# Kernel optimization log

Hardware: AMD Instinct MI355X
Metric: run time of the kernel (lower is better)

The kernel has to match this reference:

```python
import jax, jax.numpy as jnp
import numpy as np

KNN = 10       # knn_size
TOPK = 4       # top_k_select
H = 4          # num_heads
HID = 64       # edge-MLP hidden dim


def setup_inputs() -> dict:
    key = jax.random.key(0)
    ks = jax.random.split(key, 12)
    B, V, D = 4, 4096, 256
    s = 0.02
    return {
        "voxel_tokens": jax.random.normal(ks[0], (B, V, D), jnp.float32),
        "voxel_coords": jax.random.uniform(ks[1], (B, V, 3), jnp.float32) * 10.0,
        "mask": jnp.ones((B, V), dtype=bool),
        # EdgeScoringMLP: Linear(2D+3 -> 64), Linear(64 -> 1)
        "W1": jax.random.normal(ks[2], (2 * D + 3, HID), jnp.float32) * s,
        "b1": jnp.zeros((HID,), jnp.float32),
        "W2": jax.random.normal(ks[3], (HID, 1), jnp.float32) * s,
        "b2": jnp.zeros((1,), jnp.float32),
        # CrossAttention projections (D -> D)
        "Wq": jax.random.normal(ks[4], (D, D), jnp.float32) * s,
        "bq": jnp.zeros((D,), jnp.float32),
        "Wk": jax.random.normal(ks[5], (D, D), jnp.float32) * s,
        "bk": jnp.zeros((D,), jnp.float32),
        "Wv": jax.random.normal(ks[6], (D, D), jnp.float32) * s,
        "bv": jnp.zeros((D,), jnp.float32),
        "Wo": jax.random.normal(ks[7], (D, D), jnp.float32) * s,
        "bo": jnp.zeros((D,), jnp.float32),
    }


def reference(voxel_tokens, voxel_coords, mask,
              W1, b1, W2, b2, Wq, bq, Wk, bk, Wv, bv, Wo, bo):
    # mask is all-True (Vp == V per batch element), so the original per-batch
    # loop over dynamic voxel counts is an exact vmap over B. Dropouts are in
    # eval mode (identity).
    D = voxel_tokens.shape[-1]
    Dh = D // H

    def single(tok, coo):  # tok: (V, D), coo: (V, 3)
        # --- KNN graph build (squared euclidean; monotonic in true cdist) ---
        sq = jnp.sum(coo * coo, axis=-1)                        # (V,)
        d2 = sq[:, None] + sq[None, :] - 2.0 * (coo @ coo.T)    # (V, V)
        _, knn = jax.lax.top_k(-d2, KNN + 1)                    # smallest dists
        knn = knn[:, 1:]                                        # drop self, (V, KNN)

        # --- edge features: [anchor_tok, neighbor_tok, rel_pos] ---
        nb_tok = tok[knn]                                       # (V, KNN, D)
        rel = coo[knn] - coo[:, None, :]                        # (V, KNN, 3)
        anchor = jnp.broadcast_to(tok[:, None, :], nb_tok.shape)
        ef = jnp.concatenate([anchor, nb_tok, rel], axis=-1)    # (V, KNN, 2D+3)

        # --- edge-MLP scoring + softmax + top-k edge select ---
        sc = (jax.nn.relu(ef @ W1 + b1) @ W2 + b2)[..., 0]      # (V, KNN)
        aw = jax.nn.softmax(sc, axis=-1)
        _, loc = jax.lax.top_k(aw, TOPK)                        # (V, TOPK)
        sel = jnp.take_along_axis(knn, loc, axis=-1)            # (V, TOPK)
        nbr = tok[sel]                                          # (V, TOPK, D)

        # --- cross attention over selected neighbors ---
        Q = (tok @ Wq + bq).reshape(-1, H, Dh)                  # (V, H, Dh)
        K = (nbr @ Wk + bk).reshape(-1, TOPK, H, Dh)            # (V, TOPK, H, Dh)
        Vv = (nbr @ Wv + bv).reshape(-1, TOPK, H, Dh)
        att = jnp.einsum('vhd,vshd->vhs', Q, K) / jnp.sqrt(jnp.float32(Dh))
        w = jax.nn.softmax(att, axis=-1)                        # (V, H, TOPK)
        out = jnp.einsum('vhs,vshd->vhd', w, Vv).reshape(-1, D)
        return out @ Wo + bo                                    # (V, D)

    return jax.vmap(single)(voxel_tokens, voxel_coords)        # (B, V, D)
```

## Files before the change

kernel.cpp:

```cpp
#include <hip/hip_runtime.h>
#include <hip/hip_bf16.h>

#define VV 4096
#define DDIM 256
#define KNN_K 10
#define TK 4

__device__ __forceinline__ float f_sq3(float x, float y, float z) {
    return __fadd_rn(__fadd_rn(__fmul_rn(x, x), __fmul_rn(y, y)), __fmul_rn(z, z));
}
__device__ __forceinline__ float f_dot3(float ax, float ay, float az,
                                        float bx, float by, float bz) {
    float d = __fmul_rn(ax, bx);
    d = __fmaf_rn(ay, by, d);
    d = __fmaf_rn(az, bz, d);
    return d;
}

__global__ void __launch_bounds__(256) an_gemm_kernel(
    const float* __restrict__ tok,
    const float* __restrict__ W1,
    float* __restrict__ AN)
{
    __shared__ float As[16][68];
    __shared__ float Bs[16][68];

    const int mBlock = blockIdx.x * 64;
    const int grp    = blockIdx.y;
    const float* W   = W1 + (size_t)grp * 256 * 64;

    const int tid = threadIdx.x;
    const int tx = tid & 15;
    const int ty = tid >> 4;

    const int ar  = tid >> 2;
    const int ac4 = tid & 3;
    const int br  = tid >> 4;
    const int bc4 = tid & 15;

    float acc[4][4] = {};

    for (int k0 = 0; k0 < 256; k0 += 16) {
        float4 a4 = *(const float4*)&tok[(size_t)(mBlock + ar) * 256 + k0 + ac4 * 4];
        As[ac4 * 4 + 0][ar] = a4.x;
        As[ac4 * 4 + 1][ar] = a4.y;
        As[ac4 * 4 + 2][ar] = a4.z;
        As[ac4 * 4 + 3][ar] = a4.w;
        float4 b4 = *(const float4*)&W[(size_t)(k0 + br) * 64 + bc4 * 4];
        *(float4*)&Bs[br][bc4 * 4] = b4;
        __syncthreads();
        #pragma unroll
        for (int kk = 0; kk < 16; kk++) {
            float4 av = *(const float4*)&As[kk][ty * 4];
            float4 bv4 = *(const float4*)&Bs[kk][tx * 4];
            acc[0][0] = fmaf(av.x, bv4.x, acc[0][0]); acc[0][1] = fmaf(av.x, bv4.y, acc[0][1]);
            acc[0][2] = fmaf(av.x, bv4.z, acc[0][2]); acc[0][3] = fmaf(av.x, bv4.w, acc[0][3]);
            acc[1][0] = fmaf(av.y, bv4.x, acc[1][0]); acc[1][1] = fmaf(av.y, bv4.y, acc[1][1]);
            acc[1][2] = fmaf(av.y, bv4.z, acc[1][2]); acc[1][3] = fmaf(av.y, bv4.w, acc[1][3]);
            acc[2][0] = fmaf(av.z, bv4.x, acc[2][0]); acc[2][1] = fmaf(av.z, bv4.y, acc[2][1]);
            acc[2][2] = fmaf(av.z, bv4.z, acc[2][2]); acc[2][3] = fmaf(av.z, bv4.w, acc[2][3]);
            acc[3][0] = fmaf(av.w, bv4.x, acc[3][0]); acc[3][1] = fmaf(av.w, bv4.y, acc[3][1]);
            acc[3][2] = fmaf(av.w, bv4.z, acc[3][2]); acc[3][3] = fmaf(av.w, bv4.w, acc[3][3]);
        }
        __syncthreads();
    }

    #pragma unroll
    for (int i = 0; i < 4; i++) {
        int m = mBlock + ty * 4 + i;
        float4 o;
        o.x = acc[i][0]; o.y = acc[i][1]; o.z = acc[i][2]; o.w = acc[i][3];
        *(float4*)&AN[(size_t)m * 128 + grp * 64 + tx * 4] = o;
    }
}

__global__ void __launch_bounds__(256) knn_score_kernel(
    const float* __restrict__ AN,
    const float* __restrict__ coords,
    const float* __restrict__ W1,
    const float* __restrict__ b1,
    const float* __restrict__ W2,
    int* __restrict__ sel)
{
    const int q    = blockIdx.x;
    const int b    = q >> 12;
    const int v    = q & 4095;
    const int base = q & ~4095;
    const int tid  = threadIdx.x;
    const int lane = tid & 63;
    const int wave = tid >> 6;
    const float* cb = coords + (size_t)b * VV * 3;

    __shared__ float sval2[2][4];
    __shared__ int   sidx2[2][4];
    __shared__ int   sKnn[KNN_K];
    __shared__ float sA[64];
    __shared__ float sHid[KNN_K][64];
    __shared__ float sSc[KNN_K];

    const float qx = cb[v * 3 + 0];
    const float qy = cb[v * 3 + 1];
    const float qz = cb[v * 3 + 2];
    const float sqq = f_sq3(qx, qy, qz);

    if (tid < 64) sA[tid] = AN[(size_t)q * 128 + tid];

    float d2[16];
    #pragma unroll
    for (int i = 0; i < 16; i++) {
        int j = tid + i * 256;
        float xj = cb[j * 3 + 0], yj = cb[j * 3 + 1], zj = cb[j * 3 + 2];
        float sqj = f_sq3(xj, yj, zj);
        float dt  = f_dot3(qx, qy, qz, xj, yj, zj);
        d2[i] = __fsub_rn(__fadd_rn(sqq, sqj), __fmul_rn(2.0f, dt));
    }

    unsigned used = 0;
    float best = 3.4e38f;
    int   bi   = 0x7fffffff;
    #pragma unroll
    for (int i = 0; i < 16; i++) {
        if (d2[i] < best) { best = d2[i]; bi = tid + i * 256; }
    }

    for (int it = 0; it < 11; it++) {
        float rb = best;
        int   ri = bi;
        #pragma unroll
        for (int off = 1; off < 64; off <<= 1) {
            float v2 = __shfl_xor(rb, off);
            int   i2 = __shfl_xor(ri, off);
            if (v2 < rb || (v2 == rb && i2 < ri)) { rb = v2; ri = i2; }
        }
        const int p = it & 1;
        if (lane == 0) { sval2[p][wave] = rb; sidx2[p][wave] = ri; }
        __syncthreads();
        float fb = sval2[p][0]; int fi = sidx2[p][0];
        #pragma unroll
        for (int w2 = 1; w2 < 4; w2++) {
            float v2 = sval2[p][w2]; int i2 = sidx2[p][w2];
            if (v2 < fb || (v2 == fb && i2 < fi)) { fb = v2; fi = i2; }
        }
        int w = fi & 4095;
        if (it >= 1 && tid == 0) sKnn[it - 1] = w;
        if ((w & 255) == tid) {
            used |= 1u << (w >> 8);
            best = 3.4e38f; bi = 0x7fffffff;
            #pragma unroll
            for (int i = 0; i < 16; i++) {
                if (used & (1u << i)) continue;
                if (d2[i] < best) { best = d2[i]; bi = tid + i * 256; }
            }
        }
    }
    __syncthreads();

    const float qc[3] = {qx, qy, qz};
    for (int idx = tid; idx < KNN_K * 64; idx += 256) {
        int nb = idx >> 6, h = idx & 63;
        int kn = sKnn[nb];
        float acc = __fadd_rn(sA[h], AN[(size_t)(base + kn) * 128 + 64 + h]);
        #pragma unroll
        for (int c = 0; c < 3; c++) {
            float rel = __fsub_rn(cb[kn * 3 + c], qc[c]);
            acc = __fmaf_rn(rel, W1[(512 + c) * 64 + h], acc);
        }
        float hid = __fadd_rn(acc, b1[h]);
        sHid[nb][h] = hid > 0.0f ? hid : 0.0f;
    }
    __syncthreads();

    if (tid < KNN_K) {
        float s = 0.0f;
        for (int h = 0; h < 64; h++)
            s = __fmaf_rn(sHid[tid][h], W2[h], s);
        sSc[tid] = s;
    }
    __syncthreads();

    if (tid == 0) {
        unsigned um = 0;
        #pragma unroll
        for (int s = 0; s < TK; s++) {
            float bests = -3.4e38f; int bj = 0;
            for (int jj = 0; jj < KNN_K; jj++) {
                if (um & (1u << jj)) continue;
                if (sSc[jj] > bests) { bests = sSc[jj]; bj = jj; }
            }
            um |= 1u << bj;
            sel[(size_t)q * TK + s] = base + sKnn[bj];
        }
    }
}

__global__ void __launch_bounds__(256) qkv_gemm_kernel(
    const float* __restrict__ tok,
    const float* __restrict__ Wq, const float* __restrict__ bq,
    const float* __restrict__ Wk, const float* __restrict__ bk,
    const float* __restrict__ Wv, const float* __restrict__ bv,
    float* __restrict__ qkv)
{
    __shared__ float As[16][68];
    __shared__ float Bs[16][68];

    const int mBlock = blockIdx.x * 64;
    const int nBlock = blockIdx.y * 64;
    const int grp = nBlock >> 8;
    const int nIn = nBlock & 255;
    const float* W    = (grp == 0) ? Wq : (grp == 1) ? Wk : Wv;
    const float* bias = (grp == 0) ? bq : (grp == 1) ? bk : bv;

    const int tid = threadIdx.x;
    const int tx = tid & 15;
    const int ty = tid >> 4;

    const int ar  = tid >> 2;
    const int ac4 = tid & 3;
    const int br  = tid >> 4;
    const int bc4 = tid & 15;

    float acc[4][4] = {};

    for (int k0 = 0; k0 < 256; k0 += 16) {
        float4 a4 = *(const float4*)&tok[(size_t)(mBlock + ar) * 256 + k0 + ac4 * 4];
        As[ac4 * 4 + 0][ar] = a4.x;
        As[ac4 * 4 + 1][ar] = a4.y;
        As[ac4 * 4 + 2][ar] = a4.z;
        As[ac4 * 4 + 3][ar] = a4.w;
        float4 b4 = *(const float4*)&W[(size_t)(k0 + br) * 256 + nIn + bc4 * 4];
        *(float4*)&Bs[br][bc4 * 4] = b4;
        __syncthreads();
        #pragma unroll
        for (int kk = 0; kk < 16; kk++) {
            float4 av = *(const float4*)&As[kk][ty * 4];
            float4 bv4 = *(const float4*)&Bs[kk][tx * 4];
            acc[0][0] = fmaf(av.x, bv4.x, acc[0][0]); acc[0][1] = fmaf(av.x, bv4.y, acc[0][1]);
            acc[0][2] = fmaf(av.x, bv4.z, acc[0][2]); acc[0][3] = fmaf(av.x, bv4.w, acc[0][3]);
            acc[1][0] = fmaf(av.y, bv4.x, acc[1][0]); acc[1][1] = fmaf(av.y, bv4.y, acc[1][1]);
            acc[1][2] = fmaf(av.y, bv4.z, acc[1][2]); acc[1][3] = fmaf(av.y, bv4.w, acc[1][3]);
            acc[2][0] = fmaf(av.z, bv4.x, acc[2][0]); acc[2][1] = fmaf(av.z, bv4.y, acc[2][1]);
            acc[2][2] = fmaf(av.z, bv4.z, acc[2][2]); acc[2][3] = fmaf(av.z, bv4.w, acc[2][3]);
            acc[3][0] = fmaf(av.w, bv4.x, acc[3][0]); acc[3][1] = fmaf(av.w, bv4.y, acc[3][1]);
            acc[3][2] = fmaf(av.w, bv4.z, acc[3][2]); acc[3][3] = fmaf(av.w, bv4.w, acc[3][3]);
        }
        __syncthreads();
    }

    #pragma unroll
    for (int i = 0; i < 4; i++) {
        int m = mBlock + ty * 4 + i;
        float4 o;
        o.x = acc[i][0] + bias[nIn + tx * 4 + 0];
        o.y = acc[i][1] + bias[nIn + tx * 4 + 1];
        o.z = acc[i][2] + bias[nIn + tx * 4 + 2];
        o.w = acc[i][3] + bias[nIn + tx * 4 + 3];
        *(float4*)&qkv[(size_t)m * 768 + nBlock + tx * 4] = o;
    }
}

__global__ void __launch_bounds__(256) attn_gather_kernel(
    const float* __restrict__ qkv, const int* __restrict__ sel,
    float* __restrict__ attnout)
{
    const int q = blockIdx.x;
    const int tid = threadIdx.x;

    const float qv = qkv[(size_t)q * 768 + tid];

    int rows[TK];
    #pragma unroll
    for (int s = 0; s < TK; s++) rows[s] = sel[(size_t)q * TK + s];

    float att[TK];
    #pragma unroll
    for (int s = 0; s < TK; s++) {
        float p = qv * qkv[(size_t)rows[s] * 768 + 256 + tid];
        #pragma unroll
        for (int m = 1; m < 64; m <<= 1) p += __shfl_xor(p, m);
        att[s] = p * 0.125f;
    }

    float mx  = fmaxf(fmaxf(att[0], att[1]), fmaxf(att[2], att[3]));
    float e0 = expf(att[0] - mx), e1 = expf(att[1] - mx),
          e2 = expf(att[2] - mx), e3 = expf(att[3] - mx);
    float inv = 1.0f / (e0 + e1 + e2 + e3);

    float o = (e0 * qkv[(size_t)rows[0] * 768 + 512 + tid] +
               e1 * qkv[(size_t)rows[1] * 768 + 512 + tid] +
               e2 * qkv[(size_t)rows[2] * 768 + 512 + tid] +
               e3 * qkv[(size_t)rows[3] * 768 + 512 + tid]) * inv;

    attnout[(size_t)q * 256 + tid] = o;
}

__global__ void __launch_bounds__(256) wo_gemm_kernel(
    const float* __restrict__ A,
    const float* __restrict__ Wo, const float* __restrict__ bo,
    float* __restrict__ out)
{
    __shared__ float As[16][68];
    __shared__ float Bs[16][68];

    const int mBlock = blockIdx.x * 64;
    const int nBlock = blockIdx.y * 64;

    const int tid = threadIdx.x;
    const int tx = tid & 15;
    const int ty = tid >> 4;

    const int ar  = tid >> 2;
    const int ac4 = tid & 3;
    const int br  = tid >> 4;
    const int bc4 = tid & 15;

    float acc[4][4] = {};

    for (int k0 = 0; k0 < 256; k0 += 16) {
        float4 a4 = *(const float4*)&A[(size_t)(mBlock + ar) * 256 + k0 + ac4 * 4];
        As[ac4 * 4 + 0][ar] = a4.x;
        As[ac4 * 4 + 1][ar] = a4.y;
        As[ac4 * 4 + 2][ar] = a4.z;
        As[ac4 * 4 + 3][ar] = a4.w;
        float4 b4 = *(const float4*)&Wo[(size_t)(k0 + br) * 256 + nBlock + bc4 * 4];
        *(float4*)&Bs[br][bc4 * 4] = b4;
        __syncthreads();
        #pragma unroll
        for (int kk = 0; kk < 16; kk++) {
            float4 av = *(const float4*)&As[kk][ty * 4];
            float4 bv4 = *(const float4*)&Bs[kk][tx * 4];
            acc[0][0] = fmaf(av.x, bv4.x, acc[0][0]); acc[0][1] = fmaf(av.x, bv4.y, acc[0][1]);
            acc[0][2] = fmaf(av.x, bv4.z, acc[0][2]); acc[0][3] = fmaf(av.x, bv4.w, acc[0][3]);
            acc[1][0] = fmaf(av.y, bv4.x, acc[1][0]); acc[1][1] = fmaf(av.y, bv4.y, acc[1][1]);
            acc[1][2] = fmaf(av.y, bv4.z, acc[1][2]); acc[1][3] = fmaf(av.y, bv4.w, acc[1][3]);
            acc[2][0] = fmaf(av.z, bv4.x, acc[2][0]); acc[2][1] = fmaf(av.z, bv4.y, acc[2][1]);
            acc[2][2] = fmaf(av.z, bv4.z, acc[2][2]); acc[2][3] = fmaf(av.z, bv4.w, acc[2][3]);
            acc[3][0] = fmaf(av.w, bv4.x, acc[3][0]); acc[3][1] = fmaf(av.w, bv4.y, acc[3][1]);
            acc[3][2] = fmaf(av.w, bv4.z, acc[3][2]); acc[3][3] = fmaf(av.w, bv4.w, acc[3][3]);
        }
        __syncthreads();
    }

    #pragma unroll
    for (int i = 0; i < 4; i++) {
        int m = mBlock + ty * 4 + i;
        float4 o;
        o.x = acc[i][0] + bo[nBlock + tx * 4 + 0];
        o.y = acc[i][1] + bo[nBlock + tx * 4 + 1];
        o.z = acc[i][2] + bo[nBlock + tx * 4 + 2];
        o.w = acc[i][3] + bo[nBlock + tx * 4 + 3];
        *(float4*)&out[(size_t)m * 256 + nBlock + tx * 4] = o;
    }
}

__global__ void __launch_bounds__(256) fused_voxel_attn(
    const float* __restrict__ tok,
    const float* __restrict__ coords,
    const float* __restrict__ W1,
    const float* __restrict__ b1,
    const float* __restrict__ W2,
    const float* __restrict__ Wq, const float* __restrict__ bq,
    const float* __restrict__ Wk, const float* __restrict__ bk,
    const float* __restrict__ Wv, const float* __restrict__ bv,
    const float* __restrict__ Wo, const float* __restrict__ bo,
    float* __restrict__ out, int out_size)
{
    const int q    = blockIdx.x;
    const int b    = q >> 12;
    const int v    = q & 4095;
    const int base = q & ~4095;
    const int tid  = threadIdx.x;
    const float* cb = coords + (size_t)b * VV * 3;

    __shared__ float  sval[256];
    __shared__ int    sidx[256];
    __shared__ int    sKnn[KNN_K];
    __shared__ int    sSel[TK];
    __shared__ float  sTokA[DDIM];
    __shared__ float  sTokN[KNN_K][DDIM];
    __shared__ float  sAH[64];
    __shared__ float  sHid[KNN_K][64];
    __shared__ float  sSc[KNN_K];
    __shared__ float  sP[TK][256];
    __shared__ float  sAtt[4][TK];
    __shared__ float  sO[DDIM];

    const float qx = cb[v * 3 + 0];
    const float qy = cb[v * 3 + 1];
    const float qz = cb[v * 3 + 2];
    const float sqq = f_sq3(qx, qy, qz);

    float d2[16];
    #pragma unroll
    for (int i = 0; i < 16; i++) {
        int j = tid + i * 256;
        float xj = cb[j * 3 + 0], yj = cb[j * 3 + 1], zj = cb[j * 3 + 2];
        float sqj = f_sq3(xj, yj, zj);
        float dt  = f_dot3(qx, qy, qz, xj, yj, zj);
        d2[i] = __fsub_rn(__fadd_rn(sqq, sqj), __fmul_rn(2.0f, dt));
    }

    unsigned used = 0;
    for (int it = 0; it < 11; it++) {
        float best = 3.4e38f;
        int bi = 0x7fffffff;
        #pragma unroll
        for (int i = 0; i < 16; i++) {
            if (used & (1u << i)) continue;
            if (d2[i] < best) { best = d2[i]; bi = tid + i * 256; }
        }
        sval[tid] = best;
        sidx[tid] = bi;
        __syncthreads();
        for (int s = 128; s > 0; s >>= 1) {
            if (tid < s) {
                float v2 = sval[tid + s];
                int   i2 = sidx[tid + s];
                if (v2 < sval[tid] || (v2 == sval[tid] && i2 < sidx[tid])) {
                    sval[tid] = v2; sidx[tid] = i2;
                }
            }
            __syncthreads();
        }
        int w = sidx[0] & 4095;
        __syncthreads();
        if (it >= 1 && tid == 0) sKnn[it - 1] = w;
        if ((w & 255) == tid) used |= 1u << (w >> 8);
    }
    __syncthreads();

    sTokA[tid] = tok[(size_t)q * DDIM + tid];
    for (int nb = 0; nb < KNN_K; nb++)
        sTokN[nb][tid] = tok[(size_t)(base + sKnn[nb]) * DDIM + tid];
    __syncthreads();

    if (tid < 64) {
        float a = 0.0f;
        for (int k = 0; k < 256; k++)
            a = __fmaf_rn(sTokA[k], W1[k * 64 + tid], a);
        sAH[tid] = a;
    }
    __syncthreads();

    for (int idx = tid; idx < KNN_K * 64; idx += 256) {
        int nb = idx >> 6;
        int h  = idx & 63;
        float acc = sAH[h];
        const float* tn = sTokN[nb];
        for (int k = 0; k < 256; k++)
            acc = __fmaf_rn(tn[k], W1[(256 + k) * 64 + h], acc);
        #pragma unroll
        for (int c = 0; c < 3; c++) {
            float rel = __fsub_rn(cb[sKnn[nb] * 3 + c], cb[v * 3 + c]);
            acc = __fmaf_rn(rel, W1[(512 + c) * 64 + h], acc);
        }
        float hid = __fadd_rn(acc, b1[h]);
        sHid[nb][h] = hid > 0.0f ? hid : 0.0f;
    }
    __syncthreads();

    if (tid < KNN_K) {
        float s = 0.0f;
        for (int h = 0; h < 64; h++)
            s = __fmaf_rn(sHid[tid][h], W2[h], s);
        sSc[tid] = s;
    }
    __syncthreads();

    if (tid == 0) {
        unsigned um = 0;
        #pragma unroll
        for (int s = 0; s < TK; s++) {
            float best = -3.4e38f; int bj = 0;
            for (int jj = 0; jj < KNN_K; jj++) {
                if (um & (1u << jj)) continue;
                if (sSc[jj] > best) { best = sSc[jj]; bj = jj; }
            }
            um |= 1u << bj;
            sSel[s] = bj;
        }
    }
    __syncthreads();

    int ss[TK];
    float k_acc[TK], v_acc[TK];
    #pragma unroll
    for (int s = 0; s < TK; s++) {
        ss[s] = sSel[s];
        k_acc[s] = bk[tid];
        v_acc[s] = bv[tid];
    }
    float q_acc = bq[tid];

    for (int k = 0; k < 256; k++) {
        float wq = Wq[k * 256 + tid];
        float wk = Wk[k * 256 + tid];
        float wv = Wv[k * 256 + tid];
        q_acc += sTokA[k] * wq;
        #pragma unroll
        for (int s = 0; s < TK; s++) {
            float x = sTokN[ss[s]][k];
            k_acc[s] += x * wk;
            v_acc[s] += x * wv;
        }
    }

    #pragma unroll
    for (int s = 0; s < TK; s++) sP[s][tid] = q_acc * k_acc[s];
    __syncthreads();

    if (tid < 16) {
        int h = tid >> 2, s = tid & 3;
        float p = 0.0f;
        for (int d = 0; d < 64; d++) p += sP[s][h * 64 + d];
        sAtt[h][s] = p * 0.125f;
    }
    __syncthreads();

    const int hh = tid >> 6;
    float a0 = sAtt[hh][0], a1 = sAtt[hh][1], a2 = sAtt[hh][2], a3 = sAtt[hh][3];
    float mx  = fmaxf(fmaxf(a0, a1), fmaxf(a2, a3));
    float e0 = expf(a0 - mx), e1 = expf(a1 - mx), e2 = expf(a2 - mx), e3 = expf(a3 - mx);
    float inv = 1.0f / (e0 + e1 + e2 + e3);
    float o = (e0 * v_acc[0] + e1 * v_acc[1] + e2 * v_acc[2] + e3 * v_acc[3]) * inv;

    sO[tid] = o;
    __syncthreads();

    float a = bo[tid];
    for (int e = 0; e < 256; e++) a += sO[e] * Wo[e * 256 + tid];
    int oidx = q * DDIM + tid;
    if (oidx < out_size)
        out[oidx] = a;
}

extern "C" void kernel_launch(void* const* d_in, const int* in_sizes, int n_in,
                              void* d_out, int out_size, void* d_ws, size_t ws_size,
                              hipStream_t stream)
{
    const long long want[13] = {4194304LL, 49152LL, 32960LL, 64LL, 64LL,
                                65536LL, 256LL, 65536LL, 256LL,
                                65536LL, 256LL, 65536LL, 256LL};
    int idx[13];
    const int n = n_in;

    const long long* s64 = (const long long*)(const void*)in_sizes;
    const int*       s32 = in_sizes;

    bool ok = false;

    if (n >= 13 && s64[0] == want[0]) {
        ok = true;
        int walk = 0;
        for (int t = 0; t < 13; t++) {
            int f = -1;
            for (int i = walk; i < n; i++) {
                if (s64[i] == want[t]) { f = i; break; }
            }
            if (f < 0) { ok = false; break; }
            idx[t] = f; walk = f + 1;
        }
    }

    if (!ok) {
        ok = true;
        int walk = 0;
        for (int t = 0; t < 13; t++) {
            int f = -1;
            for (int i = walk; i < n; i++) {
                if ((long long)s32[i] == want[t]) { f = i; break; }
            }
            if (f < 0) { ok = false; break; }
            idx[t] = f; walk = f + 1;
        }
    }

    if (!ok) return;

    const float* tok    = (const float*)d_in[idx[0]];
    const float* coords = (const float*)d_in[idx[1]];
    const float* W1     = (const float*)d_in[idx[2]];
    const float* b1     = (const float*)d_in[idx[3]];
    const float* W2     = (const float*)d_in[idx[4]];
    const float* Wq     = (const float*)d_in[idx[5]];
    const float* bq     = (const float*)d_in[idx[6]];
    const float* Wk     = (const float*)d_in[idx[7]];
    const float* bk     = (const float*)d_in[idx[8]];
    const float* Wv     = (const float*)d_in[idx[9]];
    const float* bv     = (const float*)d_in[idx[10]];
    const float* Wo     = (const float*)d_in[idx[11]];
    const float* bo     = (const float*)d_in[idx[12]];
    float* out = (float*)d_out;

    const size_t NEED = 67371008;
    if (ws_size >= NEED) {
        char* ws = (char*)d_ws;
        int*   sel     = (int*)  (ws + 0);
        float* AN      = (float*)(ws + 262144);
        float* attnout = (float*)(ws + 262144);
        float* qkv     = (float*)(ws + 17039360);

        an_gemm_kernel<<<dim3(256, 2), dim3(256), 0, stream>>>(tok, W1, AN);
        knn_score_kernel<<<dim3(16384), dim3(256), 0, stream>>>(AN, coords, W1, b1, W2, sel);
        qkv_gemm_kernel<<<dim3(256, 12), dim3(256), 0, stream>>>(tok, Wq, bq, Wk, bk, Wv, bv, qkv);
        attn_gather_kernel<<<dim3(16384), dim3(256), 0, stream>>>(qkv, sel, attnout);
        wo_gemm_kernel<<<dim3(256, 4), dim3(256), 0, stream>>>(attnout, Wo, bo, out);
    } else {
        fused_voxel_attn<<<dim3(16384), dim3(256), 0, stream>>>(
            tok, coords, W1, b1, W2, Wq, bq, Wk, bk, Wv, bv, Wo, bo, out, out_size);
    }
}
```

Baseline: 410.4 us.

## Map one KNN query per wavefront with packed keys and top-two caching

The KNN/edge-scoring kernel now handles four queries per block, one per 64-lane wavefront, instead of one query per 256-thread block. Cross-wave shared-memory reductions and block barriers go away. Distances are packed with their indices into 64-bit sortable keys so each shuffle reduction step needs one compare. Each lane keeps only its best and second-best candidates and rescans its 64 points only when both are used. Squared norms are precomputed in the AN GEMM kernel into a new workspace buffer. The cost is more serial distance work per lane and occasional rescans that recompute distances.

After: 373.0 us. -9.1%, faster.

```diff
diff --git a/kernel.cpp b/kernel.cpp
--- a/kernel.cpp
+++ b/kernel.cpp
@@ -17,10 +17,25 @@
     return d;
 }
 
+__device__ __forceinline__ float f_d2(const float* __restrict__ cb, int j, float sqj,
+                                      float qx, float qy, float qz, float sqq) {
+    float xj = cb[j * 3 + 0], yj = cb[j * 3 + 1], zj = cb[j * 3 + 2];
+    float dt = f_dot3(qx, qy, qz, xj, yj, zj);
+    return __fsub_rn(__fadd_rn(sqq, sqj), __fmul_rn(2.0f, dt));
+}
+
+__device__ __forceinline__ unsigned long long mkkey(float d2, int j) {
+    unsigned u = __float_as_uint(d2);
+    u ^= (unsigned)((int)u >> 31) | 0x80000000u;
+    return ((unsigned long long)u << 32) | (unsigned)j;
+}
+
 __global__ void __launch_bounds__(256) an_gemm_kernel(
     const float* __restrict__ tok,
     const float* __restrict__ W1,
-    float* __restrict__ AN)
+    const float* __restrict__ coords,
+    float* __restrict__ AN,
+    float* __restrict__ sq)
 {
     __shared__ float As[16][68];
     __shared__ float Bs[16][68];
@@ -30,6 +45,12 @@
     const float* W   = W1 + (size_t)grp * 256 * 64;
 
     const int tid = threadIdx.x;
+
+    if (grp == 0 && tid < 64) {
+        int m = mBlock + tid;
+        sq[m] = f_sq3(coords[m * 3 + 0], coords[m * 3 + 1], coords[m * 3 + 2]);
+    }
+
     const int tx = tid & 15;
     const int ty = tid >> 4;
 
@@ -77,118 +98,112 @@
 __global__ void __launch_bounds__(256) knn_score_kernel(
     const float* __restrict__ AN,
     const float* __restrict__ coords,
+    const float* __restrict__ sq,
     const float* __restrict__ W1,
     const float* __restrict__ b1,
     const float* __restrict__ W2,
     int* __restrict__ sel)
 {
-    const int q    = blockIdx.x;
+    const int tid  = threadIdx.x;
+    const int lane = tid & 63;
+    const int wave = tid >> 6;
+    const int q    = blockIdx.x * 4 + wave;
     const int b    = q >> 12;
     const int v    = q & 4095;
     const int base = q & ~4095;
-    const int tid  = threadIdx.x;
-    const int lane = tid & 63;
-    const int wave = tid >> 6;
-    const float* cb = coords + (size_t)b * VV * 3;
-
-    __shared__ float sval2[2][4];
-    __shared__ int   sidx2[2][4];
-    __shared__ int   sKnn[KNN_K];
-    __shared__ float sA[64];
-    __shared__ float sHid[KNN_K][64];
-    __shared__ float sSc[KNN_K];
+    const float* cb  = coords + (size_t)b * VV * 3;
+    const float* sqb = sq + base;
+
+    __shared__ int   sKnn[4][KNN_K];
+    __shared__ float sHid[4][KNN_K][65];
+    __shared__ float sSc[4][KNN_K];
 
     const float qx = cb[v * 3 + 0];
     const float qy = cb[v * 3 + 1];
     const float qz = cb[v * 3 + 2];
     const float sqq = f_sq3(qx, qy, qz);
 
-    if (tid < 64) sA[tid] = AN[(size_t)q * 128 + tid];
-
-    float d2[16];
-    #pragma unroll
-    for (int i = 0; i < 16; i++) {
-        int j = tid + i * 256;
-        float xj = cb[j * 3 + 0], yj = cb[j * 3 + 1], zj = cb[j * 3 + 2];
-        float sqj = f_sq3(xj, yj, zj);
-        float dt  = f_dot3(qx, qy, qz, xj, yj, zj);
-        d2[i] = __fsub_rn(__fadd_rn(sqq, sqj), __fmul_rn(2.0f, dt));
-    }
-
-    unsigned used = 0;
-    float best = 3.4e38f;
-    int   bi   = 0x7fffffff;
-    #pragma unroll
-    for (int i = 0; i < 16; i++) {
-        if (d2[i] < best) { best = d2[i]; bi = tid + i * 256; }
-    }
-
+    unsigned long long best   = ~0ull;
+    unsigned long long second = ~0ull;
+    unsigned long long used   = 0ull;
+
+    #pragma unroll 4
+    for (int i = 0; i < 64; i++) {
+        int j = i * 64 + lane;
+        unsigned long long k = mkkey(f_d2(cb, j, sqb[j], qx, qy, qz, sqq), j);
+        if (k < best) { second = best; best = k; }
+        else if (k < second) { second = k; }
+    }
+
+    #pragma unroll 1
     for (int it = 0; it < 11; it++) {
-        float rb = best;
-        int   ri = bi;
+        unsigned long long rb = best;
         #pragma unroll
         for (int off = 1; off < 64; off <<= 1) {
-            float v2 = __shfl_xor(rb, off);
-            int   i2 = __shfl_xor(ri, off);
-            if (v2 < rb || (v2 == rb && i2 < ri)) { rb = v2; ri = i2; }
-        }
-        const int p = it & 1;
-        if (lane == 0) { sval2[p][wave] = rb; sidx2[p][wave] = ri; }
-        __syncthreads();
-        float fb = sval2[p][0]; int fi = sidx2[p][0];
-        #pragma unroll
-        for (int w2 = 1; w2 < 4; w2++) {
-            float v2 = sval2[p][w2]; int i2 = sidx2[p][w2];
-            if (v2 < fb || (v2 == fb && i2 < fi)) { fb = v2; fi = i2; }
-        }
-        int w = fi & 4095;
-        if (it >= 1 && tid == 0) sKnn[it - 1] = w;
-        if ((w & 255) == tid) {
-            used |= 1u << (w >> 8);
-            best = 3.4e38f; bi = 0x7fffffff;
-            #pragma unroll
-            for (int i = 0; i < 16; i++) {
-                if (used & (1u << i)) continue;
-                if (d2[i] < best) { best = d2[i]; bi = tid + i * 256; }
+            unsigned olo = __shfl_xor((unsigned)rb, off);
+            unsigned ohi = __shfl_xor((unsigned)(rb >> 32), off);
+            unsigned long long o = ((unsigned long long)ohi << 32) | olo;
+            if (o < rb) rb = o;
+        }
+        int wj = (int)((unsigned)rb & 4095u);
+        if (it >= 1 && lane == 0) sKnn[wave][it - 1] = wj;
+
+        if ((unsigned)best == (unsigned)rb) {
+            used |= 1ull << (wj >> 6);
+            best = second;
+            second = ~0ull;
+            if (best == ~0ull) {
+                #pragma unroll 1
+                for (int i = 0; i < 64; i++) {
+                    if ((used >> i) & 1ull) continue;
+                    int j = i * 64 + lane;
+                    unsigned long long k = mkkey(f_d2(cb, j, sqb[j], qx, qy, qz, sqq), j);
+                    if (k < best) { second = best; best = k; }
+                    else if (k < second) { second = k; }
+                }
             }
         }
     }
-    __syncthreads();
-
-    const float qc[3] = {qx, qy, qz};
-    for (int idx = tid; idx < KNN_K * 64; idx += 256) {
-        int nb = idx >> 6, h = idx & 63;
-        int kn = sKnn[nb];
-        float acc = __fadd_rn(sA[h], AN[(size_t)(base + kn) * 128 + 64 + h]);
-        #pragma unroll
-        for (int c = 0; c < 3; c++) {
-            float rel = __fsub_rn(cb[kn * 3 + c], qc[c]);
-            acc = __fmaf_rn(rel, W1[(512 + c) * 64 + h], acc);
-        }
-        float hid = __fadd_rn(acc, b1[h]);
-        sHid[nb][h] = hid > 0.0f ? hid : 0.0f;
-    }
-    __syncthreads();
-
-    if (tid < KNN_K) {
+
+    const float sAl = AN[(size_t)q * 128 + lane];
+    const float b1l = b1[lane];
+    const float wr0 = W1[(512 + 0) * 64 + lane];
+    const float wr1 = W1[(512 + 1) * 64 + lane];
+    const float wr2 = W1[(512 + 2) * 64 + lane];
+
+    #pragma unroll 1
+    for (int nb = 0; nb < KNN_K; nb++) {
+        int kn = sKnn[wave][nb];
+        float acc = __fadd_rn(sAl, AN[(size_t)(base + kn) * 128 + 64 + lane]);
+        float rel0 = __fsub_rn(cb[kn * 3 + 0], qx);
+        acc = __fmaf_rn(rel0, wr0, acc);
+        float rel1 = __fsub_rn(cb[kn * 3 + 1], qy);
+        acc = __fmaf_rn(rel1, wr1, acc);
+        float rel2 = __fsub_rn(cb[kn * 3 + 2], qz);
+        acc = __fmaf_rn(rel2, wr2, acc);
+        float hid = __fadd_rn(acc, b1l);
+        sHid[wave][nb][lane] = hid > 0.0f ? hid : 0.0f;
+    }
+
+    if (lane < KNN_K) {
         float s = 0.0f;
+        #pragma unroll 8
         for (int h = 0; h < 64; h++)
-            s = __fmaf_rn(sHid[tid][h], W2[h], s);
-        sSc[tid] = s;
-    }
-    __syncthreads();
-
-    if (tid == 0) {
+            s = __fmaf_rn(sHid[wave][lane][h], W2[h], s);
+        sSc[wave][lane] = s;
+    }
+
+    if (lane == 0) {
         unsigned um = 0;
         #pragma unroll
         for (int s = 0; s < TK; s++) {
             float bests = -3.4e38f; int bj = 0;
             for (int jj = 0; jj < KNN_K; jj++) {
                 if (um & (1u << jj)) continue;
-                if (sSc[jj] > bests) { bests = sSc[jj]; bj = jj; }
+                if (sSc[wave][jj] > bests) { bests = sSc[wave][jj]; bj = jj; }
             }
             um |= 1u << bj;
-            sel[(size_t)q * TK + s] = base + sKnn[bj];
+            sel[(size_t)q * TK + s] = base + sKnn[wave][bj];
         }
     }
 }
@@ -591,16 +606,17 @@
     const float* bo     = (const float*)d_in[idx[12]];
     float* out = (float*)d_out;
 
-    const size_t NEED = 67371008;
+    const size_t NEED = 67436544;
     if (ws_size >= NEED) {
         char* ws = (char*)d_ws;
         int*   sel     = (int*)  (ws + 0);
         float* AN      = (float*)(ws + 262144);
         float* attnout = (float*)(ws + 262144);
         float* qkv     = (float*)(ws + 17039360);
-
-        an_gemm_kernel<<<dim3(256, 2), dim3(256), 0, stream>>>(tok, W1, AN);
-        knn_score_kernel<<<dim3(16384), dim3(256), 0, stream>>>(AN, coords, W1, b1, W2, sel);
+        float* sq      = (float*)(ws + 67371008);
+
+        an_gemm_kernel<<<dim3(256, 2), dim3(256), 0, stream>>>(tok, W1, coords, AN, sq);
+        knn_score_kernel<<<dim3(4096), dim3(256), 0, stream>>>(AN, coords, sq, W1, b1, W2, sel);
         qkv_gemm_kernel<<<dim3(256, 12), dim3(256), 0, stream>>>(tok, Wq, bq, Wk, bk, Wv, bv, qkv);
         attn_gather_kernel<<<dim3(16384), dim3(256), 0, stream>>>(qkv, sel, attnout);
         wo_gemm_kernel<<<dim3(256, 4), dim3(256), 0, stream>>>(attnout, Wo, bo, out);
```
